# Optimization experiments

Measured on AMD Instinct MI355X. Metric: run time of the kernel, lower is better.

Reference implementation:

```python
import jax, jax.numpy as jnp
import numpy as np
from jax.scipy.linalg import expm

MS = 8  # matrix_size = sqrt(dims), dims=64


def setup_inputs() -> dict:
    key = jax.random.key(0)
    k1, k2, k3 = jax.random.split(key, 3)
    x = jax.random.normal(k1, (16384, MS), dtype=jnp.float32)
    t = jax.random.uniform(k2, (512,), dtype=jnp.float32)
    M = jax.random.normal(k3, (MS, MS), dtype=jnp.float32) * 0.01
    M0 = jnp.zeros((MS, MS), dtype=jnp.float32)
    return {"x": x, "t": t, "M": M, "M0": M0}


def reference(x, t, M, M0):
    # A = skew_symmetric(M + M0)
    B = M + M0
    A = (B - B.T) * 0.5                      # [MS, MS]
    tA = t[:, None, None] * A[None]          # [T, MS, MS]
    E = jax.vmap(expm)(tA)                   # [T, MS, MS] batched matrix exponential
    # out[t, n, i] = sum_j E[t, i, j] * x[n, j]
    out = jnp.einsum('tij,nj->tni', E, x)    # [T, N, MS]
    return out
```

## Files before the change

### kernel.cpp

```cpp
#include <hip/hip_runtime.h>

__global__ void expm_kernel(const float* __restrict__ M, const float* __restrict__ M0,
                            const float* __restrict__ t, float* __restrict__ E) {
    const int b = blockIdx.x;
    const int lane = threadIdx.x;
    const int i = lane >> 3;
    const int j = lane & 7;

    __shared__ float sA[64];
    __shared__ float sP[64];

    const float bij = M[i * 8 + j] + M0[i * 8 + j];
    const float bji = M[j * 8 + i] + M0[j * 8 + i];
    const float ta = t[b] * 0.5f * (bij - bji);

    sA[lane] = ta;
    float e = (i == j ? 1.0f : 0.0f) + ta;
    float p = ta;
    __syncthreads();

    for (int k = 2; k <= 12; ++k) {
        sP[lane] = p;
        __syncthreads();
        float s = 0.0f;
        #pragma unroll
        for (int l = 0; l < 8; ++l) {
            s = fmaf(sP[i * 8 + l], sA[l * 8 + j], s);
        }
        p = s * (1.0f / (float)k);
        e += p;
        __syncthreads();
    }

    E[b * 64 + lane] = e;
}

#define APPLY_G 8

__global__ __launch_bounds__(256) void apply_kernel(const float* __restrict__ Eall,
                                                    const float* __restrict__ x,
                                                    float* __restrict__ out,
                                                    int N) {
    const int t = blockIdx.y;

    __shared__ float sE[64];
    if (threadIdx.x < 64) sE[threadIdx.x] = Eall[t * 64 + threadIdx.x];
    __syncthreads();

    float e[64];
    #pragma unroll
    for (int c = 0; c < 64; ++c) e[c] = sE[c];

    const int n0 = blockIdx.x * (256 * APPLY_G) + threadIdx.x;
    const float4* __restrict__ x4 = (const float4*)x;
    float4* __restrict__ o4 = (float4*)(out + (size_t)t * (size_t)N * 8);

    #pragma unroll
    for (int g = 0; g < APPLY_G; ++g) {
        const int n = n0 + g * 256;
        if (n < N) {
            const float4 a = x4[2 * n];
            const float4 b = x4[2 * n + 1];
            const float xs[8] = {a.x, a.y, a.z, a.w, b.x, b.y, b.z, b.w};
            float y[8];
            #pragma unroll
            for (int ii = 0; ii < 8; ++ii) {
                float s = 0.0f;
                #pragma unroll
                for (int jj = 0; jj < 8; ++jj) {
                    s = fmaf(e[ii * 8 + jj], xs[jj], s);
                }
                y[ii] = s;
            }
            o4[2 * n]     = make_float4(y[0], y[1], y[2], y[3]);
            o4[2 * n + 1] = make_float4(y[4], y[5], y[6], y[7]);
        }
    }
}

extern "C" void kernel_launch(void* const* d_in, const int* in_sizes, int n_in,
                              void* d_out, int out_size, void* d_ws, size_t ws_size,
                              hipStream_t stream) {
    const float* x  = (const float*)d_in[0];
    const float* t  = (const float*)d_in[1];
    const float* M  = (const float*)d_in[2];
    const float* M0 = (const float*)d_in[3];
    float* out = (float*)d_out;
    float* E = (float*)d_ws;

    const int N = in_sizes[0] / 8;
    const int T = in_sizes[1];

    hipLaunchKernelGGL(expm_kernel, dim3(T), dim3(64), 0, stream, M, M0, t, E);

    const int gx = (N + 256 * APPLY_G - 1) / (256 * APPLY_G);
    hipLaunchKernelGGL(apply_kernel, dim3(gx, T), dim3(256), 0, stream, E, x, out, N);
}
```

Before: 266.5 us.

## Split each output row across two threads for coalesced float4 stores

Each thread now computes half of an 8-wide output row (4 outputs) and writes a single float4, so consecutive threads write contiguous memory. Each thread holds only half of the 8x8 matrix in registers, which lowers register pressure. Paired threads redundantly load the same x row, and per-thread work per row halves, so the loop count per thread is doubled.

```diff
diff --git a/kernel.cpp b/kernel.cpp
--- a/kernel.cpp
+++ b/kernel.cpp
@@ -35,45 +35,46 @@
     E[b * 64 + lane] = e;
 }
 
-#define APPLY_G 8
+#define APPLY_G 16
 
 __global__ __launch_bounds__(256) void apply_kernel(const float* __restrict__ Eall,
                                                     const float* __restrict__ x,
                                                     float* __restrict__ out,
                                                     int N) {
     const int t = blockIdx.y;
+    const int tid = threadIdx.x;
 
     __shared__ float sE[64];
-    if (threadIdx.x < 64) sE[threadIdx.x] = Eall[t * 64 + threadIdx.x];
+    if (tid < 64) sE[tid] = Eall[t * 64 + tid];
     __syncthreads();
 
-    float e[64];
+    const int h = tid & 1;
+    float e2[32];
     #pragma unroll
-    for (int c = 0; c < 64; ++c) e[c] = sE[c];
+    for (int c = 0; c < 32; ++c) e2[c] = sE[(h << 5) + c];
 
-    const int n0 = blockIdx.x * (256 * APPLY_G) + threadIdx.x;
+    const int S = N * 2;
+    const int s0 = blockIdx.x * (256 * APPLY_G) + tid;
     const float4* __restrict__ x4 = (const float4*)x;
     float4* __restrict__ o4 = (float4*)(out + (size_t)t * (size_t)N * 8);
 
     #pragma unroll
     for (int g = 0; g < APPLY_G; ++g) {
-        const int n = n0 + g * 256;
-        if (n < N) {
-            const float4 a = x4[2 * n];
-            const float4 b = x4[2 * n + 1];
+        const int s = s0 + g * 256;
+        if (s < S) {
+            const int sb = s & ~1;
+            const float4 a = x4[sb];
+            const float4 b = x4[sb + 1];
             const float xs[8] = {a.x, a.y, a.z, a.w, b.x, b.y, b.z, b.w};
-            float y[8];
+            float y0 = 0.0f, y1 = 0.0f, y2 = 0.0f, y3 = 0.0f;
             #pragma unroll
-            for (int ii = 0; ii < 8; ++ii) {
-                float s = 0.0f;
-                #pragma unroll
-                for (int jj = 0; jj < 8; ++jj) {
-                    s = fmaf(e[ii * 8 + jj], xs[jj], s);
-                }
-                y[ii] = s;
+            for (int jj = 0; jj < 8; ++jj) {
+                y0 = fmaf(e2[0 * 8 + jj], xs[jj], y0);
+                y1 = fmaf(e2[1 * 8 + jj], xs[jj], y1);
+                y2 = fmaf(e2[2 * 8 + jj], xs[jj], y2);
+                y3 = fmaf(e2[3 * 8 + jj], xs[jj], y3);
             }
-            o4[2 * n]     = make_float4(y[0], y[1], y[2], y[3]);
-            o4[2 * n + 1] = make_float4(y[4], y[5], y[6], y[7]);
+            o4[s] = make_float4(y0, y1, y2, y3);
         }
     }
 }
@@ -93,6 +94,7 @@
 
     hipLaunchKernelGGL(expm_kernel, dim3(T), dim3(64), 0, stream, M, M0, t, E);
 
-    const int gx = (N + 256 * APPLY_G - 1) / (256 * APPLY_G);
+    const int S = 2 * N;
+    const int gx = (S + 256 * APPLY_G - 1) / (256 * APPLY_G);
     hipLaunchKernelGGL(apply_kernel, dim3(gx, T), dim3(256), 0, stream, E, x, out, N);
 }
```

Result: no change. 269.3 us (+1.0%).

## Tile apply kernel over time steps to reuse x rows in registers

Applied to the files above, without the earlier changes.

Each apply block now loads 4 rows of x per thread into registers once and applies 8 consecutive time steps' exponential matrices, staged in shared memory, instead of handling one time step per block. This cuts repeated global reads of x across time steps and reduces the number of blocks. In exchange it uses more registers (32 x values plus 64 matrix entries) and has fewer blocks, 16x64 instead of 8x512, which may lower occupancy. The kernel is dominated by the 268MB output write, so the benefit is limited.

```diff
diff --git a/kernel.cpp b/kernel.cpp
--- a/kernel.cpp
+++ b/kernel.cpp
@@ -35,45 +35,74 @@
     E[b * 64 + lane] = e;
 }
 
-#define APPLY_G 8
+#define BLOCK 256
+#define RPT 4
+#define TBLK 8
 
-__global__ __launch_bounds__(256) void apply_kernel(const float* __restrict__ Eall,
-                                                    const float* __restrict__ x,
-                                                    float* __restrict__ out,
-                                                    int N) {
-    const int t = blockIdx.y;
+__global__ __launch_bounds__(BLOCK) void apply_kernel(const float* __restrict__ Eall,
+                                                      const float* __restrict__ x,
+                                                      float* __restrict__ out,
+                                                      int N, int T) {
+    const int tid = threadIdx.x;
+    const int n0 = blockIdx.x * (BLOCK * RPT);
+    const int t0 = blockIdx.y * TBLK;
 
-    __shared__ float sE[64];
-    if (threadIdx.x < 64) sE[threadIdx.x] = Eall[t * 64 + threadIdx.x];
+    __shared__ float sE[TBLK * 64];
+    #pragma unroll
+    for (int c = tid; c < TBLK * 64; c += BLOCK) {
+        const int t = t0 + (c >> 6);
+        sE[c] = (t < T) ? Eall[t * 64 + (c & 63)] : 0.0f;
+    }
+
+    const float4* __restrict__ x4 = (const float4*)x;
+    float xr[RPT][8];
+    bool valid[RPT];
+    #pragma unroll
+    for (int g = 0; g < RPT; ++g) {
+        const int n = n0 + g * BLOCK + tid;
+        valid[g] = (n < N);
+        if (valid[g]) {
+            const float4 a = x4[2 * n];
+            const float4 b = x4[2 * n + 1];
+            xr[g][0] = a.x; xr[g][1] = a.y; xr[g][2] = a.z; xr[g][3] = a.w;
+            xr[g][4] = b.x; xr[g][5] = b.y; xr[g][6] = b.z; xr[g][7] = b.w;
+        } else {
+            #pragma unroll
+            for (int jj = 0; jj < 8; ++jj) xr[g][jj] = 0.0f;
+        }
+    }
     __syncthreads();
 
-    float e[64];
-    #pragma unroll
-    for (int c = 0; c < 64; ++c) e[c] = sE[c];
+    for (int tt = 0; tt < TBLK; ++tt) {
+        const int t = t0 + tt;
+        if (t >= T) break;
 
-    const int n0 = blockIdx.x * (256 * APPLY_G) + threadIdx.x;
-    const float4* __restrict__ x4 = (const float4*)x;
-    float4* __restrict__ o4 = (float4*)(out + (size_t)t * (size_t)N * 8);
+        float e[64];
+        #pragma unroll
+        for (int q = 0; q < 16; ++q) {
+            const float4 v = *(const float4*)&sE[tt * 64 + q * 4];
+            e[q * 4 + 0] = v.x; e[q * 4 + 1] = v.y;
+            e[q * 4 + 2] = v.z; e[q * 4 + 3] = v.w;
+        }
 
-    #pragma unroll
-    for (int g = 0; g < APPLY_G; ++g) {
-        const int n = n0 + g * 256;
-        if (n < N) {
-            const float4 a = x4[2 * n];
-            const float4 b = x4[2 * n + 1];
-            const float xs[8] = {a.x, a.y, a.z, a.w, b.x, b.y, b.z, b.w};
-            float y[8];
-            #pragma unroll
-            for (int ii = 0; ii < 8; ++ii) {
-                float s = 0.0f;
+        float4* __restrict__ o4 = (float4*)(out + (size_t)t * (size_t)N * 8);
+        #pragma unroll
+        for (int g = 0; g < RPT; ++g) {
+            if (valid[g]) {
+                const int n = n0 + g * BLOCK + tid;
+                float y[8];
                 #pragma unroll
-                for (int jj = 0; jj < 8; ++jj) {
-                    s = fmaf(e[ii * 8 + jj], xs[jj], s);
+                for (int ii = 0; ii < 8; ++ii) {
+                    float s = 0.0f;
+                    #pragma unroll
+                    for (int jj = 0; jj < 8; ++jj) {
+                        s = fmaf(e[ii * 8 + jj], xr[g][jj], s);
+                    }
+                    y[ii] = s;
                 }
-                y[ii] = s;
+                o4[2 * n]     = make_float4(y[0], y[1], y[2], y[3]);
+                o4[2 * n + 1] = make_float4(y[4], y[5], y[6], y[7]);
             }
-            o4[2 * n]     = make_float4(y[0], y[1], y[2], y[3]);
-            o4[2 * n + 1] = make_float4(y[4], y[5], y[6], y[7]);
         }
     }
 }
@@ -93,6 +122,7 @@
 
     hipLaunchKernelGGL(expm_kernel, dim3(T), dim3(64), 0, stream, M, M0, t, E);
 
-    const int gx = (N + 256 * APPLY_G - 1) / (256 * APPLY_G);
-    hipLaunchKernelGGL(apply_kernel, dim3(gx, T), dim3(256), 0, stream, E, x, out, N);
+    const int gx = (N + BLOCK * RPT - 1) / (BLOCK * RPT);
+    const int gy = (T + TBLK - 1) / TBLK;
+    hipLaunchKernelGGL(apply_kernel, dim3(gx, gy), dim3(BLOCK), 0, stream, E, x, out, N, T);
 }
```

New measurement: 270.9 us. No clear change (+1.6%).
